# Performance work log

Measured on AMD Instinct MI355X. Metric: run time of the kernel, lower is better.

## Reference

```python
import jax, jax.numpy as jnp
import numpy as np

ALPHA, GAMMA = 0.25, 2.0
IOU_THRES = 0.5
WEIGHTS = (10.0, 10.0, 5.0, 5.0, 15.0)
MAXV = 16  # max polygon verts during quad-vs-quad clipping (<=8, padded)


def box_corners(b):
    # b: (5,) = cx, cy, w, h, theta(rad); returns (4,2) CCW corners
    cx, cy, w, h, t = b[0], b[1], b[2], b[3], b[4]
    c, s = jnp.cos(t), jnp.sin(t)
    dx = jnp.array([-0.5, 0.5, 0.5, -0.5]) * w
    dy = jnp.array([-0.5, -0.5, 0.5, 0.5]) * h
    return jnp.stack([cx + dx * c - dy * s, cy + dx * s + dy * c], axis=-1)


def pair_iou(b1, b2):
    # exact rotated-rectangle IoU via Sutherland-Hodgman clipping
    p1 = box_corners(b1)
    p2 = box_corners(b2)
    poly = jnp.zeros((MAXV, 2)).at[:4].set(p1)
    n = jnp.int32(4)
    for e in range(4):
        a = p2[e]
        d = p2[(e + 1) % 4] - a
        out = jnp.zeros((MAXV, 2))
        m = jnp.int32(0)
        for i in range(MAXV):
            cur = poly[i]
            nxt = poly[jnp.where(i + 1 >= n, 0, i + 1)]
            sc = d[0] * (cur[1] - a[1]) - d[1] * (cur[0] - a[0])
            sn = d[0] * (nxt[1] - a[1]) - d[1] * (nxt[0] - a[0])
            valid = i < n
            keep = valid & (sc >= 0)
            out = out.at[m].set(jnp.where(keep, cur, out[m]))
            m = m + keep.astype(jnp.int32)
            crossed = valid & ((sc >= 0) != (sn >= 0))
            den = sc - sn
            t = sc / jnp.where(den == 0, 1.0, den)
            ip = cur + t * (nxt - cur)
            out = out.at[m].set(jnp.where(crossed, ip, out[m]))
            m = m + crossed.astype(jnp.int32)
        poly, n = out, m
    idx = jnp.arange(MAXV)
    nxt = jnp.where(idx + 1 >= n, 0, idx + 1)
    cr = poly[:, 0] * poly[nxt, 1] - poly[nxt, 0] * poly[:, 1]
    inter = 0.5 * jnp.abs(jnp.sum(jnp.where(idx < n, cr, 0.0)))
    union = b1[2] * b1[3] + b2[2] * b2[3] - inter
    return inter / jnp.maximum(union, 1e-9)


rbox_iou_mat = jax.vmap(jax.vmap(pair_iou, (None, 0)), (0, None))  # (A,5),(G,5)->(A,G)


def min_area_square(rb):
    s = jnp.maximum(rb[:, 2], rb[:, 3])
    return jnp.stack([rb[:, 0] - s / 2, rb[:, 1] - s / 2,
                      rb[:, 0] + s / 2, rb[:, 1] + s / 2], 1)


def bbox_overlaps(a, b):
    lt = jnp.maximum(a[:, None, :2], b[None, :, :2])
    rb = jnp.minimum(a[:, None, 2:], b[None, :, 2:])
    wh = jnp.clip(rb - lt, 0.0)
    inter = wh[..., 0] * wh[..., 1]
    aa = (a[:, 2] - a[:, 0]) * (a[:, 3] - a[:, 1])
    ab = (b[:, 2] - b[:, 0]) * (b[:, 3] - b[:, 1])
    return inter / jnp.maximum(aa[:, None] + ab[None, :] - inter, 1e-9)


def encode(ex, gt):
    wx, wy, ww, wh, wt = WEIGHTS
    ew = jnp.maximum(ex[:, 2], 1.0); eh = jnp.maximum(ex[:, 3], 1.0)
    gw = jnp.maximum(gt[:, 2], 1.0); gh = jnp.maximum(gt[:, 3], 1.0)
    dx = wx * (gt[:, 0] - ex[:, 0]) / ew
    dy = wy * (gt[:, 1] - ex[:, 1]) / eh
    dw = ww * jnp.log(gw / ew)
    dh = wh * jnp.log(gh / eh)
    dt = wt * (jnp.tan(gt[:, 4]) - jnp.tan(ex[:, 4]))
    return jnp.stack([dx, dy, dw, dh, dt], 1)


def lmr5pangle(anch, dt):
    # encoded angle offset of the 90-degree-swapped box: tan(t+pi/2) = -1/tan(t)
    wt = WEIGHTS[4]
    ta = jnp.tan(anch[:, 4])
    tg = dt / wt + ta
    tg = jnp.where(jnp.abs(tg) < 1e-4, jnp.where(tg < 0, -1e-4, 1e-4), tg)
    return wt * (-1.0 / tg - ta)


def landmark_encode(ex, lm):
    wx, wy = WEIGHTS[0], WEIGHTS[1]
    ew = jnp.maximum(ex[:, 2], 1.0); eh = jnp.maximum(ex[:, 3], 1.0)
    return jnp.stack([wx * (lm[:, 0] - ex[:, 0]) / ew,
                      wy * (lm[:, 1] - ex[:, 1]) / eh,
                      wx * (lm[:, 2] - ex[:, 0]) / ew,
                      wy * (lm[:, 3] - ex[:, 1]) / eh], 1)


def smooth_l1(d, beta=1.0 / 9):
    d = jnp.abs(d)
    return jnp.where(d < beta, 0.5 * d * d / beta, d - 0.5 * beta)


def lmr5p_per_anchor(pred, tgt, anch):
    t22 = lmr5pangle(anch, pred[:, 4])
    l1 = smooth_l1(tgt[:, 0] - pred[:, 0])
    l2 = smooth_l1(tgt[:, 1] - pred[:, 1])
    l3 = smooth_l1(tgt[:, 2] - pred[:, 2])
    l4 = smooth_l1(tgt[:, 3] - pred[:, 3])
    l5 = smooth_l1(tgt[:, 2] - pred[:, 3])  # |w1 - h2|
    l6 = smooth_l1(tgt[:, 3] - pred[:, 2])  # |h1 - w2|
    l7 = smooth_l1(tgt[:, 4] - pred[:, 4])
    l8 = smooth_l1(tgt[:, 4] - t22)
    return jnp.minimum(l1 + l2 + l3 + l4 + l7, l1 + l2 + l5 + l6 + l8)


def balanced_l1(d, beta=0.5, al=0.5, ga=0.9):
    d = jnp.abs(d)
    b = np.e ** (ga / al) - 1.0
    return jnp.where(d < beta,
                     al / b * (b * d + 1.0) * jnp.log(b * d / beta + 1.0) - al * d,
                     ga * d + ga / b - al * beta)


def per_image(cls, reg, lmk, anch, ann, ls):
    valid_g = ann[:, -1] != -1.0
    has_gt = jnp.any(valid_g)
    cls = jnp.clip(cls, 1e-4, 1.0 - 1e-4)
    indicator = bbox_overlaps(min_area_square(anch), min_area_square(ann[:, :5]))
    riou = rbox_iou_mat(anch, ann[:, :5])
    ious = jnp.where(indicator >= 0.1, riou, 0.0)   # rbox_overlaps thresh=0.1 gating
    ious = jnp.where(valid_g[None, :], ious, -1.0)  # mask padded gts
    ious = jax.lax.stop_gradient(ious)              # torch computes ious on cpu numpy
    iou_max = ious.max(1)
    iou_argmax = ious.argmax(1)
    pos = iou_max >= IOU_THRES
    max_gt = ious.max(0)
    argmax_gt = ious.argmax(0)
    force = valid_g & (max_gt < IOU_THRES)
    pos = (pos.astype(jnp.int32).at[argmax_gt].max(force.astype(jnp.int32))) > 0
    num_pos = pos.sum()
    denom = jnp.maximum(num_pos.astype(cls.dtype), 1.0)
    assigned = ann[iou_argmax]                       # (A, 6)
    lab = assigned[:, -1].astype(jnp.int32)
    onehot = (lab[:, None] == jnp.arange(cls.shape[-1])[None, :]).astype(cls.dtype)
    tgt = jnp.where(pos[:, None], onehot,
                    jnp.where((iou_max < IOU_THRES - 0.1)[:, None], 0.0, -1.0))
    af = jnp.where(tgt == 1.0, ALPHA, 1.0 - ALPHA)
    fw = af * jnp.where(tgt == 1.0, 1.0 - cls, cls) ** GAMMA
    bce = -(tgt * jnp.log(cls + 1e-6) + (1.0 - tgt) * jnp.log(1.0 - cls + 1e-6))
    cls_loss = jnp.where(tgt != -1.0, fw * bce, 0.0).sum() / denom
    cls_loss = jnp.where(has_gt, cls_loss, 0.0)
    gt_safe = jnp.where(pos[:, None], assigned[:, :5], anch)  # keep masked lanes finite
    tg1 = encode(anch, gt_safe)
    r1 = jnp.where(pos, lmr5p_per_anchor(reg, tg1, anch), 0.0).sum() / (5.0 * denom)
    r1 = jnp.where(has_gt & (num_pos > 0), r1, 0.0)
    lm_safe = jnp.where(pos[:, None], ls[iou_argmax],
                        jnp.stack([anch[:, 0], anch[:, 1], anch[:, 0], anch[:, 1]], 1))
    tg2 = landmark_encode(anch, lm_safe)
    r2 = jnp.where(pos[:, None], balanced_l1(lmk - tg2), 0.0).sum() / (4.0 * denom)
    r2 = jnp.where(has_gt & (num_pos > 0), r2, 0.0)
    return cls_loss, r1, r2


def setup_inputs() -> dict:
    B, A, G, C = 2, 16384, 24, 8
    NV = 16  # valid gts per image; remaining rows padded with label -1
    ks = jax.random.split(jax.random.key(0), 16)
    classifications = jax.random.uniform(ks[0], (B, A, C), jnp.float32)
    regressions = jax.random.normal(ks[1], (B, A, 5), jnp.float32) * 0.1
    landmarks = jax.random.normal(ks[2], (B, A, 4), jnp.float32) * 0.1
    gcx = 100.0 + 800.0 * jax.random.uniform(ks[3], (B, G))
    gcy = 100.0 + 800.0 * jax.random.uniform(ks[4], (B, G))
    gw = 40.0 + 160.0 * jax.random.uniform(ks[5], (B, G))
    gh = 40.0 + 160.0 * jax.random.uniform(ks[6], (B, G))
    gth = 1.2 * jax.random.uniform(ks[7], (B, G)) - 0.6
    lab = jax.random.randint(ks[8], (B, G), 0, C).astype(jnp.float32)
    lab = jnp.where(jnp.arange(G)[None, :] >= NV, -1.0, lab)
    annotations = jnp.stack([gcx, gcy, gw, gh, gth, lab], -1)
    acx = 1024.0 * jax.random.uniform(ks[9], (B, A))
    acy = 1024.0 * jax.random.uniform(ks[10], (B, A))
    aw = 16.0 + 112.0 * jax.random.uniform(ks[11], (B, A))
    ah = 16.0 + 112.0 * jax.random.uniform(ks[12], (B, A))
    ath = 1.2 * jax.random.uniform(ks[13], (B, A)) - 0.6
    anchors = jnp.stack([acx, acy, aw, ah, ath], -1)
    # plant jittered copies of the gts so a healthy number of anchors are positive
    jit = jax.random.normal(ks[14], (B, G, 5)) * jnp.array([2.0, 2.0, 2.0, 2.0, 0.01])
    anchors = anchors.at[:, :G, :].set(annotations[:, :, :5] + jit)
    ca, sa = jnp.cos(gth), jnp.sin(gth)
    gt_linestrips = jnp.stack([gcx - 0.4 * gw * ca, gcy - 0.4 * gw * sa,
                               gcx + 0.4 * gw * ca, gcy + 0.4 * gw * sa], -1)
    return {"classifications": classifications, "regressions": regressions,
            "anchors": anchors, "annotations": annotations,
            "landmarks": landmarks, "gt_linestrips": gt_linestrips}


def reference(classifications, regressions, anchors, annotations, landmarks, gt_linestrips):
    cls_l, r1, r2 = jax.vmap(per_image)(classifications, regressions, landmarks,
                                        anchors, annotations, gt_linestrips)
    return (cls_l.mean(keepdims=True), r1.mean(keepdims=True), r2.mean(keepdims=True))
```

## Files before the change

### kernel.cpp

```cpp
#include <hip/hip_runtime.h>
#include <math.h>

#define B_N 2
#define A_N 16384
#define G_N 24
#define C_N 8
#define NV8 8
#define BPI 256
#define RECF 32
#define RECL 33

#define OFF_GTKEY  0
#define OFF_META   384
#define OFF_GTAB   512
#define OFF_AKEY   (512 + 6144)
#define OFF_PART   (OFF_AKEY + B_N * A_N * 8)

__device__ inline unsigned int fmap(float v) {
    unsigned int u = __float_as_uint(v);
    return (u & 0x80000000u) ? ~u : (u | 0x80000000u);
}
__device__ inline float funmap(unsigned int u) {
    unsigned int bits = (u & 0x80000000u) ? (u ^ 0x80000000u) : ~u;
    return __uint_as_float(bits);
}
__device__ inline unsigned long long mkkey(float v, int idx) {
    return ((unsigned long long)fmap(v) << 32) |
           (unsigned long long)(0xFFFFFFFFu - (unsigned int)idx);
}
__device__ inline float key_val(unsigned long long k) { return funmap((unsigned int)(k >> 32)); }
__device__ inline int   key_idx(unsigned long long k) { return (int)(0xFFFFFFFFu - (unsigned int)k); }

__device__ inline float smoothl1(float x) {
    const float beta = 1.0f / 9.0f;
    float d = fabsf(x);
    return (d < beta) ? (0.5f * d * d / beta) : (d - 0.5f * beta);
}
__device__ inline float balancedl1(float x) {
    const float bb  = 5.049647464412945f;
    const float alb = 0.5f / 5.049647464412945f;
    const float gab = 0.9f / 5.049647464412945f;
    float d = fabsf(x);
    if (d < 0.5f)
        return alb * (bb * d + 1.0f) * logf(bb * d / 0.5f + 1.0f) - 0.5f * d;
    return 0.9f * d + gab - 0.25f;
}
__device__ inline float focal_pos(const float* cr, int lab) {
    float s = 0.0f;
#pragma unroll
    for (int c = 0; c < C_N; c++) {
        float p = fminf(fmaxf(cr[c], 1e-4f), 0.9999f);
        if (c == lab) s += 0.25f * (1.0f - p) * (1.0f - p) * (-logf(p + 1e-6f));
        else          s += 0.75f * p * p * (-logf(1.0f - p + 1e-6f));
    }
    return s;
}
__device__ inline float focal_neg(const float* cr) {
    float s = 0.0f;
#pragma unroll
    for (int c = 0; c < C_N; c++) {
        float p = fminf(fmaxf(cr[c], 1e-4f), 0.9999f);
        s += 0.75f * p * p * (-logf(1.0f - p + 1e-6f));
    }
    return s;
}
__device__ inline float reg_loss_v(const float* rr, float acx, float acy, float aw,
                                   float ah, float ath, const float* gl) {
    float aw1 = fmaxf(aw, 1.0f), ah1 = fmaxf(ah, 1.0f);
    float gw1 = fmaxf(gl[16], 1.0f), gh1 = fmaxf(gl[17], 1.0f);
    float t1 = 10.0f * (gl[14] - acx) / aw1;
    float t2 = 10.0f * (gl[15] - acy) / ah1;
    float t3 = 5.0f * logf(gw1 / aw1);
    float t4 = 5.0f * logf(gh1 / ah1);
    float ta = tanf(ath);
    float t5 = 15.0f * (gl[20] - ta);
    float p0 = rr[0], p1 = rr[1], p2 = rr[2], p3 = rr[3], p4 = rr[4];
    float tg = p4 / 15.0f + ta;
    if (fabsf(tg) < 1e-4f) tg = (tg < 0.0f) ? -1e-4f : 1e-4f;
    float t22 = 15.0f * (-1.0f / tg - ta);
    float l1 = smoothl1(t1 - p0), l2 = smoothl1(t2 - p1);
    float l3 = smoothl1(t3 - p2), l4 = smoothl1(t4 - p3);
    float l5 = smoothl1(t3 - p3), l6 = smoothl1(t4 - p2);
    float l7 = smoothl1(t5 - p4), l8 = smoothl1(t5 - t22);
    return fminf(l1 + l2 + l3 + l4 + l7, l1 + l2 + l5 + l6 + l8);
}
__device__ inline float lmk_loss_v(const float* lk, float acx, float acy, float aw,
                                   float ah, const float* gl) {
    float aw1 = fmaxf(aw, 1.0f), ah1 = fmaxf(ah, 1.0f);
    return balancedl1(lk[0] - 10.0f * (gl[21] - acx) / aw1)
         + balancedl1(lk[1] - 10.0f * (gl[22] - acy) / ah1)
         + balancedl1(lk[2] - 10.0f * (gl[23] - acx) / aw1)
         + balancedl1(lk[3] - 10.0f * (gl[24] - acy) / ah1);
}
__device__ inline float reg_loss(const float* rr, const float* ar, const float* annr) {
    float acx = ar[0], acy = ar[1], aw = ar[2], ah = ar[3], ath = ar[4];
    float aw1 = fmaxf(aw, 1.0f), ah1 = fmaxf(ah, 1.0f);
    float gw1 = fmaxf(annr[2], 1.0f), gh1 = fmaxf(annr[3], 1.0f);
    float t1 = 10.0f * (annr[0] - acx) / aw1;
    float t2 = 10.0f * (annr[1] - acy) / ah1;
    float t3 = 5.0f * logf(gw1 / aw1);
    float t4 = 5.0f * logf(gh1 / ah1);
    float ta = tanf(ath);
    float t5 = 15.0f * (tanf(annr[4]) - ta);
    float p0 = rr[0], p1 = rr[1], p2 = rr[2], p3 = rr[3], p4 = rr[4];
    float tg = p4 / 15.0f + ta;
    if (fabsf(tg) < 1e-4f) tg = (tg < 0.0f) ? -1e-4f : 1e-4f;
    float t22 = 15.0f * (-1.0f / tg - ta);
    float l1 = smoothl1(t1 - p0), l2 = smoothl1(t2 - p1);
    float l3 = smoothl1(t3 - p2), l4 = smoothl1(t4 - p3);
    float l5 = smoothl1(t3 - p3), l6 = smoothl1(t4 - p2);
    float l7 = smoothl1(t5 - p4), l8 = smoothl1(t5 - t22);
    return fminf(l1 + l2 + l3 + l4 + l7, l1 + l2 + l5 + l6 + l8);
}
__device__ inline float lmk_loss(const float* lk, const float* ar, const float* lr) {
    float acx = ar[0], acy = ar[1];
    float aw1 = fmaxf(ar[2], 1.0f), ah1 = fmaxf(ar[3], 1.0f);
    return balancedl1(lk[0] - 10.0f * (lr[0] - acx) / aw1)
         + balancedl1(lk[1] - 10.0f * (lr[1] - acy) / ah1)
         + balancedl1(lk[2] - 10.0f * (lr[2] - acx) / aw1)
         + balancedl1(lk[3] - 10.0f * (lr[3] - acy) / ah1);
}

__global__ __launch_bounds__(64) void k_pre(
    const float* __restrict__ ann, const float* __restrict__ ls,
    float* __restrict__ gtab, unsigned long long* __restrict__ gtkey,
    int2* __restrict__ meta)
{
    int t = threadIdx.x;
    if (t < B_N * G_N) {
        const float* annr = ann + (size_t)t * 6;
        float gcx = annr[0], gcy = annr[1], gw = annr[2], gh = annr[3];
        float gth = annr[4], lab = annr[5];
        float* r = gtab + (size_t)t * RECF;
        float c2 = cosf(gth), s2 = sinf(gth);
        const float dxs[4] = {-0.5f, 0.5f, 0.5f, -0.5f};
        const float dys[4] = {-0.5f, -0.5f, 0.5f, 0.5f};
#pragma unroll
        for (int k = 0; k < 4; k++) {
            float ex = dxs[k] * gw, ey = dys[k] * gh;
            r[k]     = gcx + ex * c2 - ey * s2;
            r[4 + k] = gcy + ex * s2 + ey * c2;
        }
        r[8] = gw * gh;
        float sg = fmaxf(gw, gh);
        float gx1 = gcx - sg * 0.5f, gy1 = gcy - sg * 0.5f;
        float gx2 = gcx + sg * 0.5f, gy2 = gcy + sg * 0.5f;
        r[9] = gx1; r[10] = gy1; r[11] = gx2; r[12] = gy2;
        r[13] = (gx2 - gx1) * (gy2 - gy1);
        r[14] = gcx; r[15] = gcy; r[16] = gw; r[17] = gh; r[18] = gth; r[19] = lab;
        r[20] = tanf(gth);
        const float* lr = ls + (size_t)t * 4;
        r[21] = lr[0]; r[22] = lr[1]; r[23] = lr[2]; r[24] = lr[3];
#pragma unroll
        for (int k = 25; k < RECF; k++) r[k] = 0.0f;
        gtkey[t] = (lab != -1.0f) ? mkkey(0.0f, 0) : 0ull;
    }
    if (t < B_N * G_N && (t % G_N) == 0) {
        int b = t / G_N;
        unsigned int vm = 0; int fv = -1;
        for (int g = 0; g < G_N; g++) {
            float lab = ann[(size_t)(t + g) * 6 + 5];
            if (lab != -1.0f) { vm |= (1u << g); if (fv < 0) fv = g; }
        }
        meta[b] = make_int2((int)vm, fv);
    }
}

__global__ __launch_bounds__(64) void k_main(
    const float* __restrict__ cls, const float* __restrict__ reg,
    const float* __restrict__ anch, const float* __restrict__ lmk,
    const float* __restrict__ gtab, const int2* __restrict__ meta,
    unsigned long long* __restrict__ gtkey, unsigned long long* __restrict__ akey,
    float* __restrict__ partials)
{
    __shared__ float  glds[G_N * RECL];
    __shared__ float2 pb2[2 * NV8 * 64];
    __shared__ float  acor[9][64];
    __shared__ unsigned long long rowk[64];
    __shared__ unsigned short wl[G_N * 64];

    const int tid = threadIdx.x;
    const int b   = blockIdx.x >> 8;
    const int a   = ((blockIdx.x & (BPI - 1)) << 6) | tid;
    const size_t idx = (size_t)b * A_N + a;

    const int2 mv = meta[b];
    const float* ar = anch + idx * 5;
    float acx = ar[0], acy = ar[1], aw = ar[2], ah = ar[3], ath = ar[4];
    float4 c0 = ((const float4*)cls)[idx * 2];
    float4 c1 = ((const float4*)cls)[idx * 2 + 1];
    float crv[C_N] = {c0.x, c0.y, c0.z, c0.w, c1.x, c1.y, c1.z, c1.w};

    {
        const float4* gt4 = (const float4*)gtab + (size_t)b * G_N * (RECF / 4);
        for (int t = tid; t < G_N * (RECF / 4); t += 64) {
            float4 v = gt4[t];
            int rec = t >> 3, q = t & 7;
            float* d = glds + rec * RECL + q * 4;
            d[0] = v.x; d[1] = v.y; d[2] = v.z; d[3] = v.w;
        }
    }
    float axk[4], ayk[4];
    {
        float c1_ = cosf(ath), s1_ = sinf(ath);
        const float dxs[4] = {-0.5f, 0.5f, 0.5f, -0.5f};
        const float dys[4] = {-0.5f, -0.5f, 0.5f, 0.5f};
#pragma unroll
        for (int k = 0; k < 4; k++) {
            float dx = dxs[k] * aw, dy = dys[k] * ah;
            axk[k] = acx + dx * c1_ - dy * s1_;
            ayk[k] = acy + dx * s1_ + dy * c1_;
            acor[k][tid] = axk[k];
            acor[4 + k][tid] = ayk[k];
        }
        acor[8][tid] = aw * ah;
    }
    unsigned int validmask = (unsigned int)mv.x;
    int first_valid = mv.y;
    rowk[tid] = (first_valid >= 0) ? mkkey(0.0f, first_valid) : 0ull;
    __syncthreads();

    float sa = fmaxf(aw, ah);
    float ax1 = acx - sa * 0.5f, ay1 = acy - sa * 0.5f;
    float ax2 = acx + sa * 0.5f, ay2 = acy + sa * 0.5f;
    float areaA = (ax2 - ax1) * (ay2 - ay1);

    int cnt = 0;
    for (unsigned int vm = validmask; vm; vm &= vm - 1) {
        int g = __ffs((int)vm) - 1;
        const float* gq = glds + g * RECL;
        float iw = fmaxf(fminf(ax2, gq[11]) - fmaxf(ax1, gq[9]), 0.0f);
        float ih = fmaxf(fminf(ay2, gq[12]) - fmaxf(ay1, gq[10]), 0.0f);
        float inter0 = iw * ih;
        float ind = inter0 / fmaxf(areaA + gq[13] - inter0, 1e-9f);
        bool pass = (ind >= 0.1f);
        unsigned long long bal = __ballot(pass);
        if (pass) {
            int off = __popcll(bal & ((1ull << tid) - 1ull));
            wl[cnt + off] = (unsigned short)((tid << 5) | g);
        }
        cnt += __popcll(bal);
    }
    __syncthreads();

    for (int i = tid; i < cnt; i += 64) {
        unsigned int e = wl[i];
        int owner = (int)(e >> 5);
        int g = (int)(e & 31u);
        const float* gl = glds + g * RECL;
        float p2x[4], p2y[4];
#pragma unroll
        for (int k = 0; k < 4; k++) { p2x[k] = gl[k]; p2y[k] = gl[4 + k]; }
        float ax_[4], ay_[4];
#pragma unroll
        for (int k = 0; k < 4; k++) { ax_[k] = acor[k][owner]; ay_[k] = acor[4 + k][owner]; }

        int n;
        {
            float apx = p2x[0], apy = p2y[0];
            float dxe = p2x[1] - apx, dye = p2y[1] - apy;
            int m = 0;
#pragma unroll
            for (int v = 0; v < 4; v++) {
                float cx_ = ax_[v], cy_ = ay_[v];
                float nx_ = ax_[(v + 1) & 3], ny_ = ay_[(v + 1) & 3];
                float sc = dxe * (cy_ - apy) - dye * (cx_ - apx);
                float sn = dxe * (ny_ - apy) - dye * (nx_ - apx);
                bool ci = (sc >= 0.0f), niv = (sn >= 0.0f);
                if (ci) {
                    if (m < NV8) pb2[(0 * NV8 + m) * 64 + tid] = make_float2(cx_, cy_);
                    m++;
                }
                if (ci != niv) {
                    float den = sc - sn;
                    float t = sc / ((den == 0.0f) ? 1.0f : den);
                    if (m < NV8) pb2[(0 * NV8 + m) * 64 + tid] =
                        make_float2(cx_ + t * (nx_ - cx_), cy_ + t * (ny_ - cy_));
                    m++;
                }
            }
            n = m;
        }
        for (int eidx = 1; eidx <= 2; eidx++) {
            int src = (eidx == 1) ? 0 : 1;
            int dst = (eidx == 1) ? 1 : 0;
            float apx = p2x[eidx], apy = p2y[eidx];
            float dxe = p2x[(eidx + 1) & 3] - apx, dye = p2y[(eidx + 1) & 3] - apy;
            int m = 0;
            if (n > 0) {
                float2 first = pb2[(src * NV8 + 0) * 64 + tid];
                float2 cur = first;
                float2 pref = (n > 1) ? pb2[(src * NV8 + 1) * 64 + tid] : first;
                for (int v = 0; v < n; v++) {
                    float2 nxt = (v + 1 < n) ? pref : first;
                    if (v + 2 < n) pref = pb2[(src * NV8 + v + 2) * 64 + tid];
                    float sc = dxe * (cur.y - apy) - dye * (cur.x - apx);
                    float sn = dxe * (nxt.y - apy) - dye * (nxt.x - apx);
                    bool ci = (sc >= 0.0f), niv = (sn >= 0.0f);
                    if (ci) {
                        if (m < NV8) pb2[(dst * NV8 + m) * 64 + tid] = cur;
                        m++;
                    }
                    if (ci != niv) {
                        float den = sc - sn;
                        float t = sc / ((den == 0.0f) ? 1.0f : den);
                        if (m < NV8) pb2[(dst * NV8 + m) * 64 + tid] =
                            make_float2(cur.x + t * (nxt.x - cur.x), cur.y + t * (nxt.y - cur.y));
                        m++;
                    }
                    cur = nxt;
                }
            }
            n = m;
        }
        float ssum = 0.0f;
        {
            float apx = p2x[3], apy = p2y[3];
            float dxe = p2x[0] - apx, dye = p2y[0] - apy;
            float2 efirst = make_float2(0.0f, 0.0f), eprev = efirst;
            int fcnt = 0;
            if (n > 0) {
                float2 first = pb2[(0 * NV8 + 0) * 64 + tid];
                float2 cur = first;
                float2 pref = (n > 1) ? pb2[(0 * NV8 + 1) * 64 + tid] : first;
                for (int v = 0; v < n; v++) {
                    float2 nxt = (v + 1 < n) ? pref : first;
                    if (v + 2 < n) pref = pb2[(0 * NV8 + v + 2) * 64 + tid];
                    float sc = dxe * (cur.y - apy) - dye * (cur.x - apx);
                    float sn = dxe * (nxt.y - apy) - dye * (nxt.x - apx);
                    bool ci = (sc >= 0.0f), niv = (sn >= 0.0f);
                    if (ci) {
                        if (fcnt == 0) efirst = cur;
                        else ssum += eprev.x * cur.y - cur.x * eprev.y;
                        eprev = cur; fcnt++;
                    }
                    if (ci != niv) {
                        float den = sc - sn;
                        float t = sc / ((den == 0.0f) ? 1.0f : den);
                        float2 ip = make_float2(cur.x + t * (nxt.x - cur.x),
                                                cur.y + t * (nxt.y - cur.y));
                        if (fcnt == 0) efirst = ip;
                        else ssum += eprev.x * ip.y - ip.x * eprev.y;
                        eprev = ip; fcnt++;
                    }
                    cur = nxt;
                }
            }
            if (fcnt > 0) ssum += eprev.x * efirst.y - efirst.x * eprev.y;
        }
        float interA = 0.5f * fabsf(ssum);
        float uni = acor[8][owner] + gl[8] - interA;
        float val = interA / fmaxf(uni, 1e-9f);

        atomicMax(&rowk[owner], mkkey(val, g));
        if (val > 0.0f) {
            int aowner = ((blockIdx.x & (BPI - 1)) << 6) | owner;
            atomicMax(&gtkey[b * G_N + g], mkkey(val, aowner));
        }
    }
    __syncthreads();

    unsigned long long rowkey = rowk[tid];
    akey[idx] = rowkey;

    float iou_max = key_val(rowkey);
    int gmax = key_idx(rowkey);
    float cls_sum = 0.0f, reg_sum = 0.0f, lmk_sum = 0.0f;
    int pc = 0;
    if (iou_max >= 0.5f) {
        const float* gl = glds + gmax * RECL;
        pc = 1;
        cls_sum = focal_pos(crv, (int)gl[19]);
        reg_sum = reg_loss_v(reg + idx * 5, acx, acy, aw, ah, ath, gl);
        lmk_sum = lmk_loss_v(lmk + idx * 4, acx, acy, aw, ah, gl);
    } else if (iou_max < 0.4f) {
        cls_sum = focal_neg(crv);
    }

    float fpc = (float)pc;
    for (int off = 32; off; off >>= 1) {
        cls_sum += __shfl_down(cls_sum, off);
        reg_sum += __shfl_down(reg_sum, off);
        lmk_sum += __shfl_down(lmk_sum, off);
        fpc     += __shfl_down(fpc, off);
    }
    if (tid == 0) {
        float* p = partials + (size_t)blockIdx.x * 4;
        p[0] = cls_sum; p[1] = reg_sum; p[2] = lmk_sum; p[3] = fpc;
    }
}

__global__ __launch_bounds__(128) void k_fix(
    const float* __restrict__ cls, const float* __restrict__ reg,
    const float* __restrict__ anch, const float* __restrict__ ann,
    const float* __restrict__ lmk, const float* __restrict__ ls,
    const unsigned long long* __restrict__ gtkey, const unsigned long long* __restrict__ akey,
    const float* __restrict__ partials, float* __restrict__ out)
{
    __shared__ float res[B_N][3];
    const int tid = threadIdx.x;
    const int b = tid >> 6, lane = tid & 63;

    double s0 = 0.0, s1 = 0.0, s2 = 0.0, s3 = 0.0;
    for (int r = lane; r < BPI; r += 64) {
        const float* p = partials + (size_t)(b * BPI + r) * 4;
        s0 += p[0]; s1 += p[1]; s2 += p[2]; s3 += p[3];
    }
    for (int off = 32; off; off >>= 1) {
        s0 += __shfl_down(s0, off);
        s1 += __shfl_down(s1, off);
        s2 += __shfl_down(s2, off);
        s3 += __shfl_down(s3, off);
    }

    const float* annb = ann + (size_t)b * G_N * 6;
    float dc = 0.0f, dr = 0.0f, dl = 0.0f; int dn = 0;
    if (lane < G_N) {
        bool valid = annb[lane * 6 + 5] != -1.0f;
        unsigned long long k = gtkey[b * G_N + lane];
        int fa = key_idx(k);
        bool force = valid && (key_val(k) < 0.5f);
        if (force) {
            for (int g2 = 0; g2 < lane; g2++) {
                if (annb[g2 * 6 + 5] == -1.0f) continue;
                unsigned long long k2 = gtkey[b * G_N + g2];
                if (key_val(k2) < 0.5f && key_idx(k2) == fa) { force = false; break; }
            }
        }
        if (force) {
            size_t fidx = (size_t)b * A_N + fa;
            unsigned long long ak = akey[fidx];
            float im = key_val(ak);
            if (!(im >= 0.5f)) {
                dn = 1;
                int gm = key_idx(ak);
                const float* cr = cls + fidx * C_N;
                float crv[C_N];
#pragma unroll
                for (int c = 0; c < C_N; c++) crv[c] = cr[c];
                const float* annr = annb + gm * 6;
                const float* arr = anch + fidx * 5;
                dc = focal_pos(crv, (int)annr[5]);
                if (im < 0.4f) dc -= focal_neg(crv);
                dr = reg_loss(reg + fidx * 5, arr, annr);
                dl = lmk_loss(lmk + fidx * 4, arr, ls + (size_t)(b * G_N + gm) * 4);
            }
        }
    }
    float fdn = (float)dn;
    for (int off = 32; off; off >>= 1) {
        dc  += __shfl_down(dc, off);
        dr  += __shfl_down(dr, off);
        dl  += __shfl_down(dl, off);
        fdn += __shfl_down(fdn, off);
    }
    if (lane == 0) {
        bool has_gt = false;
        for (int g = 0; g < G_N; g++)
            if (annb[g * 6 + 5] != -1.0f) has_gt = true;
        float np = (float)s3 + fdn;
        float denom = fmaxf(np, 1.0f);
        res[b][0] = has_gt ? (float)((s0 + dc) / denom) : 0.0f;
        res[b][1] = (has_gt && np > 0.0f) ? (float)((s1 + dr) / (5.0 * denom)) : 0.0f;
        res[b][2] = (has_gt && np > 0.0f) ? (float)((s2 + dl) / (4.0 * denom)) : 0.0f;
    }
    __syncthreads();
    if (tid == 0) {
        out[0] = (res[0][0] + res[1][0]) * 0.5f;
        out[1] = (res[0][1] + res[1][1]) * 0.5f;
        out[2] = (res[0][2] + res[1][2]) * 0.5f;
    }
}

extern "C" void kernel_launch(void* const* d_in, const int* in_sizes, int n_in,
                              void* d_out, int out_size, void* d_ws, size_t ws_size,
                              hipStream_t stream)
{
    (void)in_sizes; (void)n_in; (void)out_size; (void)ws_size;
    const float* cls  = (const float*)d_in[0];
    const float* reg  = (const float*)d_in[1];
    const float* anch = (const float*)d_in[2];
    const float* ann  = (const float*)d_in[3];
    const float* lmk  = (const float*)d_in[4];
    const float* ls   = (const float*)d_in[5];

    char* ws = (char*)d_ws;
    unsigned long long* gtkey = (unsigned long long*)(ws + OFF_GTKEY);
    int2*  meta  = (int2*)(ws + OFF_META);
    float* gtab  = (float*)(ws + OFF_GTAB);
    unsigned long long* akey = (unsigned long long*)(ws + OFF_AKEY);
    float* partials = (float*)(ws + OFF_PART);
    float* out = (float*)d_out;

    hipLaunchKernelGGL(k_pre, dim3(1), dim3(64), 0, stream, ann, ls, gtab, gtkey, meta);
    hipLaunchKernelGGL(k_main, dim3(B_N * BPI), dim3(64), 0, stream,
                       cls, reg, anch, lmk, gtab, meta, gtkey, akey, partials);
    hipLaunchKernelGGL(k_fix, dim3(1), dim3(128), 0, stream,
                       cls, reg, anch, ann, lmk, ls, gtkey, akey, partials, out);
}
```

Before: 104.6 us.

## Fold GT preprocessing into main kernel and replace global column atomics with per-block partials

Removes the single-thread-block preprocessing kernel. Each main block now computes the GT table and the valid mask itself, using a ballot. Per-GT column max keys are accumulated with shared-memory atomics and written out per block, instead of global 64-bit atomicMax. The fix kernel grows to 384 threads to reduce these per-block column keys. Regression and landmark loads are also hoisted early. This saves one launch and global atomic contention, at the cost of redundant per-block trig work and an extra reduction pass.

```diff
diff --git a/kernel.cpp b/kernel.cpp
--- a/kernel.cpp
+++ b/kernel.cpp
@@ -7,13 +7,10 @@
 #define C_N 8
 #define NV8 8
 #define BPI 256
-#define RECF 32
 #define RECL 33
 
-#define OFF_GTKEY  0
-#define OFF_META   384
-#define OFF_GTAB   512
-#define OFF_AKEY   (512 + 6144)
+#define OFF_GCOL   0
+#define OFF_AKEY   (512 * G_N * 8)
 #define OFF_PART   (OFF_AKEY + B_N * A_N * 8)
 
 __device__ inline unsigned int fmap(float v) {
@@ -121,62 +118,18 @@
          + balancedl1(lk[3] - 10.0f * (lr[3] - acy) / ah1);
 }
 
-__global__ __launch_bounds__(64) void k_pre(
-    const float* __restrict__ ann, const float* __restrict__ ls,
-    float* __restrict__ gtab, unsigned long long* __restrict__ gtkey,
-    int2* __restrict__ meta)
-{
-    int t = threadIdx.x;
-    if (t < B_N * G_N) {
-        const float* annr = ann + (size_t)t * 6;
-        float gcx = annr[0], gcy = annr[1], gw = annr[2], gh = annr[3];
-        float gth = annr[4], lab = annr[5];
-        float* r = gtab + (size_t)t * RECF;
-        float c2 = cosf(gth), s2 = sinf(gth);
-        const float dxs[4] = {-0.5f, 0.5f, 0.5f, -0.5f};
-        const float dys[4] = {-0.5f, -0.5f, 0.5f, 0.5f};
-#pragma unroll
-        for (int k = 0; k < 4; k++) {
-            float ex = dxs[k] * gw, ey = dys[k] * gh;
-            r[k]     = gcx + ex * c2 - ey * s2;
-            r[4 + k] = gcy + ex * s2 + ey * c2;
-        }
-        r[8] = gw * gh;
-        float sg = fmaxf(gw, gh);
-        float gx1 = gcx - sg * 0.5f, gy1 = gcy - sg * 0.5f;
-        float gx2 = gcx + sg * 0.5f, gy2 = gcy + sg * 0.5f;
-        r[9] = gx1; r[10] = gy1; r[11] = gx2; r[12] = gy2;
-        r[13] = (gx2 - gx1) * (gy2 - gy1);
-        r[14] = gcx; r[15] = gcy; r[16] = gw; r[17] = gh; r[18] = gth; r[19] = lab;
-        r[20] = tanf(gth);
-        const float* lr = ls + (size_t)t * 4;
-        r[21] = lr[0]; r[22] = lr[1]; r[23] = lr[2]; r[24] = lr[3];
-#pragma unroll
-        for (int k = 25; k < RECF; k++) r[k] = 0.0f;
-        gtkey[t] = (lab != -1.0f) ? mkkey(0.0f, 0) : 0ull;
-    }
-    if (t < B_N * G_N && (t % G_N) == 0) {
-        int b = t / G_N;
-        unsigned int vm = 0; int fv = -1;
-        for (int g = 0; g < G_N; g++) {
-            float lab = ann[(size_t)(t + g) * 6 + 5];
-            if (lab != -1.0f) { vm |= (1u << g); if (fv < 0) fv = g; }
-        }
-        meta[b] = make_int2((int)vm, fv);
-    }
-}
-
 __global__ __launch_bounds__(64) void k_main(
     const float* __restrict__ cls, const float* __restrict__ reg,
-    const float* __restrict__ anch, const float* __restrict__ lmk,
-    const float* __restrict__ gtab, const int2* __restrict__ meta,
-    unsigned long long* __restrict__ gtkey, unsigned long long* __restrict__ akey,
+    const float* __restrict__ anch, const float* __restrict__ ann,
+    const float* __restrict__ lmk, const float* __restrict__ ls,
+    unsigned long long* __restrict__ gcol, unsigned long long* __restrict__ akey,
     float* __restrict__ partials)
 {
     __shared__ float  glds[G_N * RECL];
     __shared__ float2 pb2[2 * NV8 * 64];
     __shared__ float  acor[9][64];
     __shared__ unsigned long long rowk[64];
+    __shared__ unsigned long long colk[G_N];
     __shared__ unsigned short wl[G_N * 64];
 
     const int tid = threadIdx.x;
@@ -184,23 +137,51 @@
     const int a   = ((blockIdx.x & (BPI - 1)) << 6) | tid;
     const size_t idx = (size_t)b * A_N + a;
 
-    const int2 mv = meta[b];
     const float* ar = anch + idx * 5;
     float acx = ar[0], acy = ar[1], aw = ar[2], ah = ar[3], ath = ar[4];
     float4 c0 = ((const float4*)cls)[idx * 2];
     float4 c1 = ((const float4*)cls)[idx * 2 + 1];
+    const float* rr = reg + idx * 5;
+    float rv[5] = {rr[0], rr[1], rr[2], rr[3], rr[4]};
+    float4 lv = ((const float4*)lmk)[idx];
+    float an0 = 0, an1 = 0, an2 = 0, an3 = 0, an4 = 0, an5 = -1.0f;
+    float ls0 = 0, ls1 = 0, ls2 = 0, ls3 = 0;
+    if (tid < G_N) {
+        const float* annr = ann + (size_t)(b * G_N + tid) * 6;
+        an0 = annr[0]; an1 = annr[1]; an2 = annr[2];
+        an3 = annr[3]; an4 = annr[4]; an5 = annr[5];
+        const float* lr = ls + (size_t)(b * G_N + tid) * 4;
+        ls0 = lr[0]; ls1 = lr[1]; ls2 = lr[2]; ls3 = lr[3];
+    }
     float crv[C_N] = {c0.x, c0.y, c0.z, c0.w, c1.x, c1.y, c1.z, c1.w};
 
-    {
-        const float4* gt4 = (const float4*)gtab + (size_t)b * G_N * (RECF / 4);
-        for (int t = tid; t < G_N * (RECF / 4); t += 64) {
-            float4 v = gt4[t];
-            int rec = t >> 3, q = t & 7;
-            float* d = glds + rec * RECL + q * 4;
-            d[0] = v.x; d[1] = v.y; d[2] = v.z; d[3] = v.w;
-        }
-    }
-    float axk[4], ayk[4];
+    if (tid < G_N) {
+        float* r = glds + tid * RECL;
+        float c2 = cosf(an4), s2 = sinf(an4);
+        const float dxs[4] = {-0.5f, 0.5f, 0.5f, -0.5f};
+        const float dys[4] = {-0.5f, -0.5f, 0.5f, 0.5f};
+#pragma unroll
+        for (int k = 0; k < 4; k++) {
+            float ex = dxs[k] * an2, ey = dys[k] * an3;
+            r[k]     = an0 + ex * c2 - ey * s2;
+            r[4 + k] = an1 + ex * s2 + ey * c2;
+        }
+        r[8] = an2 * an3;
+        float sg = fmaxf(an2, an3);
+        float gx1 = an0 - sg * 0.5f, gy1 = an1 - sg * 0.5f;
+        float gx2 = an0 + sg * 0.5f, gy2 = an1 + sg * 0.5f;
+        r[9] = gx1; r[10] = gy1; r[11] = gx2; r[12] = gy2;
+        r[13] = (gx2 - gx1) * (gy2 - gy1);
+        r[14] = an0; r[15] = an1; r[16] = an2; r[17] = an3; r[18] = an4; r[19] = an5;
+        r[20] = tanf(an4);
+        r[21] = ls0; r[22] = ls1; r[23] = ls2; r[24] = ls3;
+        colk[tid] = 0ull;
+    }
+    unsigned int validmask =
+        (unsigned int)__ballot(tid < G_N && an5 != -1.0f);
+    int first_valid = validmask ? (__ffs((int)validmask) - 1) : -1;
+    rowk[tid] = (first_valid >= 0) ? mkkey(0.0f, first_valid) : 0ull;
+
     {
         float c1_ = cosf(ath), s1_ = sinf(ath);
         const float dxs[4] = {-0.5f, 0.5f, 0.5f, -0.5f};
@@ -208,16 +189,11 @@
 #pragma unroll
         for (int k = 0; k < 4; k++) {
             float dx = dxs[k] * aw, dy = dys[k] * ah;
-            axk[k] = acx + dx * c1_ - dy * s1_;
-            ayk[k] = acy + dx * s1_ + dy * c1_;
-            acor[k][tid] = axk[k];
-            acor[4 + k][tid] = ayk[k];
+            acor[k][tid]     = acx + dx * c1_ - dy * s1_;
+            acor[4 + k][tid] = acy + dx * s1_ + dy * c1_;
         }
         acor[8][tid] = aw * ah;
     }
-    unsigned int validmask = (unsigned int)mv.x;
-    int first_valid = mv.y;
-    rowk[tid] = (first_valid >= 0) ? mkkey(0.0f, first_valid) : 0ull;
     __syncthreads();
 
     float sa = fmaxf(aw, ah);
@@ -355,10 +331,13 @@
         atomicMax(&rowk[owner], mkkey(val, g));
         if (val > 0.0f) {
             int aowner = ((blockIdx.x & (BPI - 1)) << 6) | owner;
-            atomicMax(&gtkey[b * G_N + g], mkkey(val, aowner));
+            atomicMax(&colk[g], mkkey(val, aowner));
         }
     }
     __syncthreads();
+
+    if (tid < G_N)
+        gcol[(size_t)blockIdx.x * G_N + tid] = colk[tid];
 
     unsigned long long rowkey = rowk[tid];
     akey[idx] = rowkey;
@@ -371,8 +350,9 @@
         const float* gl = glds + gmax * RECL;
         pc = 1;
         cls_sum = focal_pos(crv, (int)gl[19]);
-        reg_sum = reg_loss_v(reg + idx * 5, acx, acy, aw, ah, ath, gl);
-        lmk_sum = lmk_loss_v(lmk + idx * 4, acx, acy, aw, ah, gl);
+        reg_sum = reg_loss_v(rv, acx, acy, aw, ah, ath, gl);
+        float lkv[4] = {lv.x, lv.y, lv.z, lv.w};
+        lmk_sum = lmk_loss_v(lkv, acx, acy, aw, ah, gl);
     } else if (iou_max < 0.4f) {
         cls_sum = focal_neg(crv);
     }
@@ -390,40 +370,66 @@
     }
 }
 
-__global__ __launch_bounds__(128) void k_fix(
+__global__ __launch_bounds__(384) void k_fix(
     const float* __restrict__ cls, const float* __restrict__ reg,
     const float* __restrict__ anch, const float* __restrict__ ann,
     const float* __restrict__ lmk, const float* __restrict__ ls,
-    const unsigned long long* __restrict__ gtkey, const unsigned long long* __restrict__ akey,
+    const unsigned long long* __restrict__ gcol, const unsigned long long* __restrict__ akey,
     const float* __restrict__ partials, float* __restrict__ out)
 {
+    __shared__ unsigned long long colpart[B_N * G_N * 8];
+    __shared__ unsigned long long colfin[B_N * G_N];
     __shared__ float res[B_N][3];
     const int tid = threadIdx.x;
-    const int b = tid >> 6, lane = tid & 63;
+    const int b = (tid >> 6) & 1, lane = tid & 63;
 
     double s0 = 0.0, s1 = 0.0, s2 = 0.0, s3 = 0.0;
-    for (int r = lane; r < BPI; r += 64) {
-        const float* p = partials + (size_t)(b * BPI + r) * 4;
-        s0 += p[0]; s1 += p[1]; s2 += p[2]; s3 += p[3];
-    }
-    for (int off = 32; off; off >>= 1) {
-        s0 += __shfl_down(s0, off);
-        s1 += __shfl_down(s1, off);
-        s2 += __shfl_down(s2, off);
-        s3 += __shfl_down(s3, off);
-    }
+    if (tid < 128) {
+        for (int r = lane; r < BPI; r += 64) {
+            const float* p = partials + (size_t)(b * BPI + r) * 4;
+            s0 += p[0]; s1 += p[1]; s2 += p[2]; s3 += p[3];
+        }
+        for (int off = 32; off; off >>= 1) {
+            s0 += __shfl_down(s0, off);
+            s1 += __shfl_down(s1, off);
+            s2 += __shfl_down(s2, off);
+            s3 += __shfl_down(s3, off);
+        }
+    }
+
+    {
+        int pair = tid >> 3, sub = tid & 7;
+        int pb = pair / G_N, g = pair - pb * G_N;
+        unsigned long long k = mkkey(0.0f, 0);
+        for (int r = sub; r < BPI; r += 8) {
+            unsigned long long v = gcol[(size_t)(pb * BPI + r) * G_N + g];
+            if (v > k) k = v;
+        }
+        colpart[pair * 8 + sub] = k;
+    }
+    __syncthreads();
+    if (tid < B_N * G_N) {
+        unsigned long long k = colpart[tid * 8];
+#pragma unroll
+        for (int s = 1; s < 8; s++) {
+            unsigned long long v = colpart[tid * 8 + s];
+            if (v > k) k = v;
+        }
+        colfin[tid] = k;
+    }
+    __syncthreads();
 
     const float* annb = ann + (size_t)b * G_N * 6;
     float dc = 0.0f, dr = 0.0f, dl = 0.0f; int dn = 0;
-    if (lane < G_N) {
+    if (tid < 128 && lane < G_N) {
         bool valid = annb[lane * 6 + 5] != -1.0f;
-        unsigned long long k = gtkey[b * G_N + lane];
+        unsigned long long k = colfin[b * G_N + lane];
         int fa = key_idx(k);
         bool force = valid && (key_val(k) < 0.5f);
         if (force) {
             for (int g2 = 0; g2 < lane; g2++) {
                 if (annb[g2 * 6 + 5] == -1.0f) continue;
-                unsigned long long k2 = gtkey[b * G_N + g2];
+                unsigned long long k2 = colfin[b * G_N + g2];
                 if (key_val(k2) < 0.5f && key_idx(k2) == fa) { force = false; break; }
             }
         }
@@ -447,22 +453,24 @@
             }
         }
     }
-    float fdn = (float)dn;
-    for (int off = 32; off; off >>= 1) {
-        dc  += __shfl_down(dc, off);
-        dr  += __shfl_down(dr, off);
-        dl  += __shfl_down(dl, off);
-        fdn += __shfl_down(fdn, off);
-    }
-    if (lane == 0) {
-        bool has_gt = false;
-        for (int g = 0; g < G_N; g++)
-            if (annb[g * 6 + 5] != -1.0f) has_gt = true;
-        float np = (float)s3 + fdn;
-        float denom = fmaxf(np, 1.0f);
-        res[b][0] = has_gt ? (float)((s0 + dc) / denom) : 0.0f;
-        res[b][1] = (has_gt && np > 0.0f) ? (float)((s1 + dr) / (5.0 * denom)) : 0.0f;
-        res[b][2] = (has_gt && np > 0.0f) ? (float)((s2 + dl) / (4.0 * denom)) : 0.0f;
+    if (tid < 128) {
+        float fdn = (float)dn;
+        for (int off = 32; off; off >>= 1) {
+            dc  += __shfl_down(dc, off);
+            dr  += __shfl_down(dr, off);
+            dl  += __shfl_down(dl, off);
+            fdn += __shfl_down(fdn, off);
+        }
+        if (lane == 0) {
+            bool has_gt = false;
+            for (int g = 0; g < G_N; g++)
+                if (annb[g * 6 + 5] != -1.0f) has_gt = true;
+            float np = (float)s3 + fdn;
+            float denom = fmaxf(np, 1.0f);
+            res[b][0] = has_gt ? (float)((s0 + dc) / denom) : 0.0f;
+            res[b][1] = (has_gt && np > 0.0f) ? (float)((s1 + dr) / (5.0 * denom)) : 0.0f;
+            res[b][2] = (has_gt && np > 0.0f) ? (float)((s2 + dl) / (4.0 * denom)) : 0.0f;
+        }
     }
     __syncthreads();
     if (tid == 0) {
@@ -485,16 +493,13 @@
     const float* ls   = (const float*)d_in[5];
 
     char* ws = (char*)d_ws;
-    unsigned long long* gtkey = (unsigned long long*)(ws + OFF_GTKEY);
-    int2*  meta  = (int2*)(ws + OFF_META);
-    float* gtab  = (float*)(ws + OFF_GTAB);
+    unsigned long long* gcol = (unsigned long long*)(ws + OFF_GCOL);
     unsigned long long* akey = (unsigned long long*)(ws + OFF_AKEY);
     float* partials = (float*)(ws + OFF_PART);
     float* out = (float*)d_out;
 
-    hipLaunchKernelGGL(k_pre, dim3(1), dim3(64), 0, stream, ann, ls, gtab, gtkey, meta);
     hipLaunchKernelGGL(k_main, dim3(B_N * BPI), dim3(64), 0, stream,
-                       cls, reg, anch, lmk, gtab, meta, gtkey, akey, partials);
-    hipLaunchKernelGGL(k_fix, dim3(1), dim3(128), 0, stream,
-                       cls, reg, anch, ann, lmk, ls, gtkey, akey, partials, out);
-}
+                       cls, reg, anch, ann, lmk, ls, gcol, akey, partials);
+    hipLaunchKernelGGL(k_fix, dim3(1), dim3(384), 0, stream,
+                       cls, reg, anch, ann, lmk, ls, gcol, akey, partials, out);
+}
```

Result: faster. 87.81 us, median of 2 (-16.1%).
